# Kernel optimization log

Measured on AMD Instinct MI355X. Metric: run time of the kernel, lower is better.

Reference implementation:

```python
import jax, jax.numpy as jnp
import numpy as np

NUM_HEADS = 16
HEAD_DIM = 64
MAX_TIME = 10000


def apply_rope(x):
    """Interleaved RoPE, faithful to apply_rotary_encoding with the _rope_kernel.

    The NxN kernel maps pairs (x0, x1) -> (-x1, x0); we do it with a reshape
    instead of the dense matmul for efficiency (same math).
    x: [b, t, h, d]
    """
    b, t, h, d = x.shape
    pos = jnp.arange(t, dtype=jnp.float32)                         # [t]
    freq_seq = jnp.arange(d // 2, dtype=jnp.float32) / (d // 2)
    inv_freq = jnp.repeat(jnp.float32(MAX_TIME) ** (-freq_seq), 2)  # [d], interleaved
    theta = pos[:, None] * inv_freq[None, :]                        # [t, d]
    pairs = x.reshape(b, t, h, d // 2, 2)
    x_rot = jnp.stack([-pairs[..., 1], pairs[..., 0]], axis=-1).reshape(b, t, h, d)
    cos = jnp.cos(theta).astype(x.dtype)[None, :, None, :]
    sin = jnp.sin(theta).astype(x.dtype)[None, :, None, :]
    return x * cos + x_rot * sin


def setup_inputs() -> dict:
    key = jax.random.key(0)
    ks = jax.random.split(key, 6)
    B, T, E = 8, 1024, 1024
    H = NUM_HEADS * HEAD_DIM
    s = 0.02  # typical init scale for bias-free Linear weights
    return {
        "inputs_q": jax.random.normal(ks[0], (B, T, E), jnp.float32),
        "inputs_kv": jax.random.normal(ks[1], (B, T, E), jnp.float32),
        "w_q": jax.random.normal(ks[2], (E, H), jnp.float32) * s,
        "w_k": jax.random.normal(ks[3], (E, H), jnp.float32) * s,
        "w_v": jax.random.normal(ks[4], (E, H), jnp.float32) * s,
        "w_o": jax.random.normal(ks[5], (H, E), jnp.float32) * s,
    }


def reference(inputs_q, inputs_kv, w_q, w_k, w_v, w_o):
    b, t, e = inputs_q.shape
    q = (inputs_q @ w_q).reshape(b, t, NUM_HEADS, HEAD_DIM)   # [b,t,h,d]
    k = (inputs_kv @ w_k).reshape(b, -1, NUM_HEADS, HEAD_DIM)  # [b,T,h,d]
    v = (inputs_kv @ w_v).reshape(b, -1, NUM_HEADS, HEAD_DIM)
    q = apply_rope(q)
    k = apply_rope(k)
    logits = jnp.einsum('bthd,bThd->bhtT', q, k) * (1.0 / jnp.sqrt(jnp.float32(HEAD_DIM)))
    attn = jax.nn.softmax(logits, axis=-1)                    # [b,h,t,T]
    out = jnp.einsum('bhtT,bThd->bthd', attn, v).reshape(b, t, NUM_HEADS * HEAD_DIM)
    return out @ w_o                                          # [b,t,e]
```

## Files before the change

kernel.cpp:

```cpp
#include <hip/hip_runtime.h>
#include <math.h>


typedef __attribute__((ext_vector_type(8))) short bf16x8;
typedef __attribute__((ext_vector_type(4))) float f32x4;
typedef __attribute__((ext_vector_type(16))) float f32x16;

__device__ __forceinline__ ushort f2bf(float f) {
    union { float f; uint32_t u; } v; v.f = f;
    uint32_t r = (v.u + 0x7FFF + ((v.u >> 16) & 1)) >> 16;
    return (ushort)r;
}
__device__ __forceinline__ uint cvt_pk_bf16(float a, float b) {
    uint r;
    asm("v_cvt_pk_bf16_f32 %0, %1, %2" : "=v"(r) : "v"(a), "v"(b));
    return r;
}
__device__ __forceinline__ float bf2f(ushort u) {
    union { uint32_t u; float f; } v; v.u = ((uint32_t)u) << 16;
    return v.f;
}

__device__ __forceinline__ void gload16(const ushort* g, ushort* l) {
    __builtin_amdgcn_global_load_lds(
        (const __attribute__((address_space(1))) unsigned int*)g,
        (__attribute__((address_space(3))) unsigned int*)l, 16, 0, 0);
}

__global__ void cast_bf16_2(const float* __restrict__ X0, ushort* __restrict__ Y0,
                            const float* __restrict__ X1, ushort* __restrict__ Y1)
{
    const float* X = blockIdx.y ? X1 : X0;
    ushort* Y = blockIdx.y ? Y1 : Y0;
    int i = blockIdx.x * 256 + threadIdx.x;
    float4 a = ((const float4*)X)[2 * i];
    float4 b = ((const float4*)X)[2 * i + 1];
    union { float4 f; ushort u[8]; } o;
    o.u[0] = f2bf(a.x); o.u[1] = f2bf(a.y); o.u[2] = f2bf(a.z); o.u[3] = f2bf(a.w);
    o.u[4] = f2bf(b.x); o.u[5] = f2bf(b.y); o.u[6] = f2bf(b.z); o.u[7] = f2bf(b.w);
    ((float4*)Y)[i] = o.f;
}

__global__ void transpose_cast_4(const float* __restrict__ w0, ushort* __restrict__ t0,
                                 const float* __restrict__ w1, ushort* __restrict__ t1,
                                 const float* __restrict__ w2, ushort* __restrict__ t2,
                                 const float* __restrict__ w3, ushort* __restrict__ t3)
{
    const int z = blockIdx.z;
    const float* W = (z == 0) ? w0 : (z == 1) ? w1 : (z == 2) ? w2 : w3;
    ushort* Wt = (z == 0) ? t0 : (z == 1) ? t1 : (z == 2) ? t2 : t3;
    __shared__ float t[32][33];
    int bx = blockIdx.x * 32, by = blockIdx.y * 32;
    int tx = threadIdx.x, ty = threadIdx.y;
#pragma unroll
    for (int e = 0; e < 32; e += 8)
        t[ty + e][tx] = W[(size_t)(by + ty + e) * 1024 + bx + tx];
    __syncthreads();
#pragma unroll
    for (int e = 0; e < 32; e += 8)
        Wt[(size_t)(bx + ty + e) * 1024 + by + tx] = f2bf(t[tx][ty + e]);
}

template <bool F32OUT>
__global__ __launch_bounds__(256, 2)
void gemm_bf16(const ushort* __restrict__ A, const ushort* __restrict__ Bt,
               void* __restrict__ C, int M, int N, int K)
{
    __shared__ ushort As[2][128 * 32];
    __shared__ ushort Bs[2][128 * 32];
    const int tid = threadIdx.x;
    const int w = tid >> 6, l = tid & 63;
    const int row0 = blockIdx.x * 128, col0 = blockIdx.y * 128;
    const int wr = (w >> 1) * 64, wc = (w & 1) * 64;

    f32x4 acc[4][4];
#pragma unroll
    for (int i = 0; i < 4; ++i)
#pragma unroll
        for (int j = 0; j < 4; ++j) acc[i][j] = (f32x4)0.f;

    const ushort* Ag = A + (size_t)(row0 + w * 32 + (l >> 2)) * K + (l & 3) * 8;
    const ushort* Bg = Bt + (size_t)(col0 + w * 32 + (l >> 2)) * K + (l & 3) * 8;

    const int arow = (wr + (l & 15)) * 32;
    const int brow = (wc + (l & 15)) * 32;
    const int koff = (l >> 4) * 8;

    auto STAGE = [&](int buf, int kt) {
        ushort* Asw = &As[buf][w * 1024];
        ushort* Bsw = &Bs[buf][w * 1024];
        gload16(Ag + kt, Asw);
        gload16(Ag + 16 * K + kt, Asw + 512);
        gload16(Bg + kt, Bsw);
        gload16(Bg + 16 * K + kt, Bsw + 512);
    };
    auto COMPUTE = [&](int buf) {
        bf16x8 af[4], bfr[4];
#pragma unroll
        for (int fm = 0; fm < 4; ++fm)
            af[fm] = *(const bf16x8*)&As[buf][arow + fm * 512 + koff];
#pragma unroll
        for (int fn = 0; fn < 4; ++fn)
            bfr[fn] = *(const bf16x8*)&Bs[buf][brow + fn * 512 + koff];
#pragma unroll
        for (int fm = 0; fm < 4; ++fm)
#pragma unroll
            for (int fn = 0; fn < 4; ++fn)
                acc[fm][fn] = __builtin_amdgcn_mfma_f32_16x16x32_bf16(
                    af[fm], bfr[fn], acc[fm][fn], 0, 0, 0);
    };

    STAGE(0, 0);
    asm volatile("s_waitcnt vmcnt(0)" ::: "memory");
    __builtin_amdgcn_s_barrier();
    int cur = 0;
    for (int kt = 32; kt < K; kt += 32) {
        STAGE(cur ^ 1, kt);
        COMPUTE(cur);
        asm volatile("s_waitcnt vmcnt(0)" ::: "memory");
        __builtin_amdgcn_s_barrier();
        cur ^= 1;
    }
    COMPUTE(cur);

    const int crow = (l >> 4) * 4;
    const int ccol = l & 15;
#pragma unroll
    for (int fm = 0; fm < 4; ++fm)
#pragma unroll
        for (int fn = 0; fn < 4; ++fn)
#pragma unroll
            for (int r = 0; r < 4; ++r) {
                size_t row = row0 + wr + fm * 16 + crow + r;
                size_t col = col0 + wc + fn * 16 + ccol;
                if (F32OUT)
                    ((float*)C)[row * N + col] = acc[fm][fn][r];
                else
                    ((ushort*)C)[row * N + col] = f2bf(acc[fm][fn][r]);
            }
}

__global__ void rope_bf16_2(ushort* __restrict__ Qb, ushort* __restrict__ Kb)
{
    ushort* X = blockIdx.y ? Kb : Qb;
    const float scale = blockIdx.y ? 1.0f : 0.125f;
    int idx = blockIdx.x * 256 + threadIdx.x;
    int pc = idx & 511;
    int t = (idx >> 9) & 1023;
    int i = pc & 31;
    float inv_freq = exp2f(-(float)i * (13.28771238f / 32.0f));
    float theta = (float)t * inv_freq;
    float s, c;
    sincosf(theta, &s, &c);
    uint32_t v = ((uint32_t*)X)[idx];
    float x0 = bf2f((ushort)(v & 0xffff));
    float x1 = bf2f((ushort)(v >> 16));
    float o0 = (x0 * c - x1 * s) * scale;
    float o1 = (x1 * c + x0 * s) * scale;
    ((uint32_t*)X)[idx] = (uint32_t)f2bf(o0) | ((uint32_t)f2bf(o1) << 16);
}

__global__ __launch_bounds__(256, 4)
void attn_bf16_v2(const ushort* __restrict__ Q, const ushort* __restrict__ K,
                  const ushort* __restrict__ V, ushort* __restrict__ O)
{
    __shared__ uint Ksu[64 * 34];
    __shared__ uint Vtu[64 * 34];
    __shared__ uint Os[4][32 * 36];

    const int tid = threadIdx.x;
    const int w = tid >> 6, l = tid & 63;
    const int lo = l & 31, hi = l >> 5;
    const int bid = blockIdx.x;
    const int qt = bid >> 7;
    const int hb = bid & 127;
    const int h = hb >> 3, b = hb & 7;
    const int colh = h * 64;

    const size_t qrow = (size_t)(b * 1024 + qt * 128 + w * 32 + lo);
    bf16x8 qb[4];
#pragma unroll
    for (int kc = 0; kc < 4; ++kc)
        qb[kc] = *(const bf16x8*)&Q[qrow * 1024 + colh + kc * 16 + hi * 8];

    f32x16 acc[2];
#pragma unroll
    for (int i = 0; i < 2; ++i) acc[i] = (f32x16)0.f;
    float lsum = 0.f;

    const size_t kvbase = (size_t)b * 1024 * 1024 + colh;

    const int skey = tid >> 3, sc = tid & 7;
    const int kp = tid & 31, vg = tid >> 5;

    for (int kt = 0; kt < 16; ++kt) {
        __syncthreads();
#pragma unroll
        for (int u = 0; u < 2; ++u) {
            int key = skey + u * 32;
            uint4 kv = *(const uint4*)&K[kvbase + (size_t)(kt * 64 + key) * 1024 + sc * 8];
            *(uint2*)&Ksu[key * 34 + sc * 4] = make_uint2(kv.x, kv.y);
            *(uint2*)&Ksu[key * 34 + sc * 4 + 2] = make_uint2(kv.z, kv.w);
        }
        {
            uint4 va = *(const uint4*)&V[kvbase + (size_t)(kt * 64 + 2 * kp) * 1024 + vg * 8];
            uint4 vb = *(const uint4*)&V[kvbase + (size_t)(kt * 64 + 2 * kp + 1) * 1024 + vg * 8];
            const ushort* pa = (const ushort*)&va;
            const ushort* pb = (const ushort*)&vb;
#pragma unroll
            for (int e = 0; e < 8; ++e)
                Vtu[(vg * 8 + e) * 34 + kp] = (uint)pa[e] | ((uint)pb[e] << 16);
        }
        __syncthreads();

        uint pw[16];
#pragma unroll
        for (int mt = 0; mt < 2; ++mt) {
            f32x16 s = (f32x16)0.f;
            const int rbase = (mt * 32 + lo) * 34 + hi * 4;
#pragma unroll
            for (int kc = 0; kc < 4; ++kc) {
                union { uint2 d[2]; bf16x8 v; } ak;
                ak.d[0] = *(const uint2*)&Ksu[rbase + kc * 8];
                ak.d[1] = *(const uint2*)&Ksu[rbase + kc * 8 + 2];
                s = __builtin_amdgcn_mfma_f32_32x32x16_bf16(ak.v, qb[kc], s, 0, 0, 0);
            }
            float p[16];
#pragma unroll
            for (int r = 0; r < 16; ++r) {
                p[r] = __expf(s[r]);
                lsum += p[r];
            }
#pragma unroll
            for (int rp = 0; rp < 8; ++rp)
                pw[mt * 8 + rp] = cvt_pk_bf16(p[2 * rp], p[2 * rp + 1]);
        }

        bf16x8 pf[4];
#pragma unroll
        for (int mt = 0; mt < 2; ++mt) {
            uint* W = &pw[mt * 8];
            uint e0 = (uint)__shfl_xor((int)(hi ? W[0] : W[2]), 32);
            uint e1 = (uint)__shfl_xor((int)(hi ? W[1] : W[3]), 32);
            uint e2 = (uint)__shfl_xor((int)(hi ? W[4] : W[6]), 32);
            uint e3 = (uint)__shfl_xor((int)(hi ? W[5] : W[7]), 32);
            union { uint u[4]; bf16x8 v; } f0, f1;
            if (hi == 0) {
                f0.u[0] = W[0]; f0.u[1] = W[1]; f0.u[2] = e0; f0.u[3] = e1;
                f1.u[0] = W[4]; f1.u[1] = W[5]; f1.u[2] = e2; f1.u[3] = e3;
            } else {
                f0.u[0] = e0; f0.u[1] = e1; f0.u[2] = W[2]; f0.u[3] = W[3];
                f1.u[0] = e2; f1.u[1] = e3; f1.u[2] = W[6]; f1.u[3] = W[7];
            }
            pf[mt * 2 + 0] = f0.v;
            pf[mt * 2 + 1] = f1.v;
        }

#pragma unroll
        for (int dmt = 0; dmt < 2; ++dmt) {
            const int rbase = (dmt * 32 + lo) * 34 + hi * 4;
#pragma unroll
            for (int kcg = 0; kcg < 4; ++kcg) {
                union { uint2 d[2]; bf16x8 v; } vk;
                vk.d[0] = *(const uint2*)&Vtu[rbase + kcg * 8];
                vk.d[1] = *(const uint2*)&Vtu[rbase + kcg * 8 + 2];
                acc[dmt] = __builtin_amdgcn_mfma_f32_32x32x16_bf16(vk.v, pf[kcg], acc[dmt], 0, 0, 0);
            }
        }
    }

    float tot = lsum + __shfl_xor(lsum, 32);
    float inv = 1.0f / tot;

    uint* Osw = &Os[w][0];
#pragma unroll
    for (int dmt = 0; dmt < 2; ++dmt)
#pragma unroll
        for (int rp = 0; rp < 8; ++rp) {
            float a0 = acc[dmt][2 * rp] * inv;
            float a1 = acc[dmt][2 * rp + 1] * inv;
            Osw[lo * 36 + dmt * 16 + (rp & 1) + 4 * (rp >> 1) + 2 * hi] =
                cvt_pk_bf16(a0, a1);
        }
    __builtin_amdgcn_s_waitcnt(0);
#pragma unroll
    for (int u = 0; u < 4; ++u) {
        int slot = l + u * 64;
        int qr = slot >> 3, c = slot & 7;
        float4 val = *(const float4*)&Osw[qr * 36 + c * 4];
        *(float4*)&O[(size_t)(b * 1024 + qt * 128 + w * 32 + qr) * 1024 + colh + c * 8] = val;
    }
}

extern "C" void kernel_launch(void* const* d_in, const int* in_sizes, int n_in,
                              void* d_out, int out_size, void* d_ws, size_t ws_size,
                              hipStream_t stream)
{
    const float* xq  = (const float*)d_in[0];
    const float* xkv = (const float*)d_in[1];
    const float* wq  = (const float*)d_in[2];
    const float* wk  = (const float*)d_in[3];
    const float* wv  = (const float*)d_in[4];
    const float* wo  = (const float*)d_in[5];
    float* out = (float*)d_out;

    const int M = 8192, N = 1024, Kd = 1024;
    ushort* Aq  = (ushort*)d_ws;
    ushort* Akv = Aq  + 8388608;
    ushort* WqT = Akv + 8388608;
    ushort* WkT = WqT + 1048576;
    ushort* WvT = WkT + 1048576;
    ushort* WoT = WvT + 1048576;
    ushort* Qb  = WoT + 1048576;
    ushort* Kb  = Qb  + 8388608;
    ushort* Vb  = Kb  + 8388608;
    ushort* Ob  = Vb  + 8388608;

    cast_bf16_2<<<dim3(4096, 2), 256, 0, stream>>>(xq, Aq, xkv, Akv);
    transpose_cast_4<<<dim3(32, 32, 4), dim3(32, 8), 0, stream>>>(
        wq, WqT, wk, WkT, wv, WvT, wo, WoT);

    dim3 gg(M / 128, N / 128);
    gemm_bf16<false><<<gg, 256, 0, stream>>>(Aq,  WqT, Qb, M, N, Kd);
    gemm_bf16<false><<<gg, 256, 0, stream>>>(Akv, WkT, Kb, M, N, Kd);
    gemm_bf16<false><<<gg, 256, 0, stream>>>(Akv, WvT, Vb, M, N, Kd);

    rope_bf16_2<<<dim3(16384, 2), 256, 0, stream>>>(Qb, Kb);

    attn_bf16_v2<<<1024, 256, 0, stream>>>(Qb, Kb, Vb, Ob);

    gemm_bf16<true><<<gg, 256, 0, stream>>>(Ob, WoT, (void*)out, M, N, Kd);
}
```

Measured before the change: 193.1 us.

## Fuse QKV GEMMs into one launch with RoPE epilogue and exp2 softmax

Merges the three Q/K/V projection GEMMs into a single launch over a 3x grid, relying on the transposed weights and outputs being contiguous in the workspace. It applies RoPE and the Q scale (folded with log2e) in the GEMM epilogue using lane shuffles, and the attention kernel switches to exp2f. This removes the separate RoPE pass over Q and K and two kernel launches, and gives the merged GEMM more blocks to fill the device. The cost is extra sincos work in the epilogue and a higher launch-bounds occupancy target.

```diff
diff --git a/kernel.cpp b/kernel.cpp
--- a/kernel.cpp
+++ b/kernel.cpp
@@ -5,6 +5,9 @@
 typedef __attribute__((ext_vector_type(8))) short bf16x8;
 typedef __attribute__((ext_vector_type(4))) float f32x4;
 typedef __attribute__((ext_vector_type(16))) float f32x16;
+
+#define LOG2E 1.44269504f
+#define QSCALE (0.125f * LOG2E)
 
 __device__ __forceinline__ ushort f2bf(float f) {
     union { float f; uint32_t u; } v; v.f = f;
@@ -61,17 +64,22 @@
         Wt[(size_t)(bx + ty + e) * 1024 + by + tx] = f2bf(t[tx][ty + e]);
 }
 
-template <bool F32OUT>
-__global__ __launch_bounds__(256, 2)
-void gemm_bf16(const ushort* __restrict__ A, const ushort* __restrict__ Bt,
-               void* __restrict__ C, int M, int N, int K)
-{
+__global__ __launch_bounds__(256, 4)
+void gemm_qkv(const ushort* __restrict__ Aq, const ushort* __restrict__ Akv,
+              const ushort* __restrict__ Wt, ushort* __restrict__ Out)
+{
+    const int K = 1024, N = 1024;
     __shared__ ushort As[2][128 * 32];
     __shared__ ushort Bs[2][128 * 32];
     const int tid = threadIdx.x;
     const int w = tid >> 6, l = tid & 63;
-    const int row0 = blockIdx.x * 128, col0 = blockIdx.y * 128;
+    const int mat = blockIdx.y >> 3;
+    const int row0 = blockIdx.x * 128, col0 = (blockIdx.y & 7) * 128;
     const int wr = (w >> 1) * 64, wc = (w & 1) * 64;
+
+    const ushort* A = mat ? Akv : Aq;
+    const ushort* Bt = Wt + (size_t)mat * (1024 * 1024);
+    ushort* C = Out + (size_t)mat * 8388608;
 
     f32x4 acc[4][4];
 #pragma unroll
@@ -125,6 +133,34 @@
 
     const int crow = (l >> 4) * 4;
     const int ccol = l & 15;
+
+    if (mat < 2) {
+        const float scale = (mat == 0) ? QSCALE : 1.0f;
+        float invf[4];
+#pragma unroll
+        for (int fn = 0; fn < 4; ++fn) {
+            int i = (fn * 16 + ccol) >> 1;
+            invf[fn] = exp2f(-(float)i * (13.28771238f / 32.0f));
+        }
+        const int odd = ccol & 1;
+#pragma unroll
+        for (int fm = 0; fm < 4; ++fm)
+#pragma unroll
+            for (int r = 0; r < 4; ++r) {
+                int t = (row0 + wr + fm * 16 + crow + r) & 1023;
+#pragma unroll
+                for (int fn = 0; fn < 4; ++fn) {
+                    float x = acc[fm][fn][r];
+                    float partner = __shfl_xor(x, 1, 64);
+                    float sv, cv;
+                    sincosf((float)t * invf[fn], &sv, &cv);
+                    float o = odd ? fmaf(partner, sv, x * cv)
+                                  : fmaf(-partner, sv, x * cv);
+                    acc[fm][fn][r] = o * scale;
+                }
+            }
+    }
+
 #pragma unroll
     for (int fm = 0; fm < 4; ++fm)
 #pragma unroll
@@ -133,31 +169,83 @@
             for (int r = 0; r < 4; ++r) {
                 size_t row = row0 + wr + fm * 16 + crow + r;
                 size_t col = col0 + wc + fn * 16 + ccol;
-                if (F32OUT)
-                    ((float*)C)[row * N + col] = acc[fm][fn][r];
-                else
-                    ((ushort*)C)[row * N + col] = f2bf(acc[fm][fn][r]);
-            }
-}
-
-__global__ void rope_bf16_2(ushort* __restrict__ Qb, ushort* __restrict__ Kb)
-{
-    ushort* X = blockIdx.y ? Kb : Qb;
-    const float scale = blockIdx.y ? 1.0f : 0.125f;
-    int idx = blockIdx.x * 256 + threadIdx.x;
-    int pc = idx & 511;
-    int t = (idx >> 9) & 1023;
-    int i = pc & 31;
-    float inv_freq = exp2f(-(float)i * (13.28771238f / 32.0f));
-    float theta = (float)t * inv_freq;
-    float s, c;
-    sincosf(theta, &s, &c);
-    uint32_t v = ((uint32_t*)X)[idx];
-    float x0 = bf2f((ushort)(v & 0xffff));
-    float x1 = bf2f((ushort)(v >> 16));
-    float o0 = (x0 * c - x1 * s) * scale;
-    float o1 = (x1 * c + x0 * s) * scale;
-    ((uint32_t*)X)[idx] = (uint32_t)f2bf(o0) | ((uint32_t)f2bf(o1) << 16);
+                C[row * N + col] = f2bf(acc[fm][fn][r]);
+            }
+}
+
+__global__ __launch_bounds__(256, 2)
+void gemm_out(const ushort* __restrict__ A, const ushort* __restrict__ Bt,
+              float* __restrict__ C, int M, int N, int K)
+{
+    __shared__ ushort As[2][128 * 32];
+    __shared__ ushort Bs[2][128 * 32];
+    const int tid = threadIdx.x;
+    const int w = tid >> 6, l = tid & 63;
+    const int row0 = blockIdx.x * 128, col0 = blockIdx.y * 128;
+    const int wr = (w >> 1) * 64, wc = (w & 1) * 64;
+
+    f32x4 acc[4][4];
+#pragma unroll
+    for (int i = 0; i < 4; ++i)
+#pragma unroll
+        for (int j = 0; j < 4; ++j) acc[i][j] = (f32x4)0.f;
+
+    const ushort* Ag = A + (size_t)(row0 + w * 32 + (l >> 2)) * K + (l & 3) * 8;
+    const ushort* Bg = Bt + (size_t)(col0 + w * 32 + (l >> 2)) * K + (l & 3) * 8;
+
+    const int arow = (wr + (l & 15)) * 32;
+    const int brow = (wc + (l & 15)) * 32;
+    const int koff = (l >> 4) * 8;
+
+    auto STAGE = [&](int buf, int kt) {
+        ushort* Asw = &As[buf][w * 1024];
+        ushort* Bsw = &Bs[buf][w * 1024];
+        gload16(Ag + kt, Asw);
+        gload16(Ag + 16 * K + kt, Asw + 512);
+        gload16(Bg + kt, Bsw);
+        gload16(Bg + 16 * K + kt, Bsw + 512);
+    };
+    auto COMPUTE = [&](int buf) {
+        bf16x8 af[4], bfr[4];
+#pragma unroll
+        for (int fm = 0; fm < 4; ++fm)
+            af[fm] = *(const bf16x8*)&As[buf][arow + fm * 512 + koff];
+#pragma unroll
+        for (int fn = 0; fn < 4; ++fn)
+            bfr[fn] = *(const bf16x8*)&Bs[buf][brow + fn * 512 + koff];
+#pragma unroll
+        for (int fm = 0; fm < 4; ++fm)
+#pragma unroll
+            for (int fn = 0; fn < 4; ++fn)
+                acc[fm][fn] = __builtin_amdgcn_mfma_f32_16x16x32_bf16(
+                    af[fm], bfr[fn], acc[fm][fn], 0, 0, 0);
+    };
+
+    STAGE(0, 0);
+    asm volatile("s_waitcnt vmcnt(0)" ::: "memory");
+    __builtin_amdgcn_s_barrier();
+    int cur = 0;
+    for (int kt = 32; kt < K; kt += 32) {
+        STAGE(cur ^ 1, kt);
+        COMPUTE(cur);
+        asm volatile("s_waitcnt vmcnt(0)" ::: "memory");
+        __builtin_amdgcn_s_barrier();
+        cur ^= 1;
+    }
+    COMPUTE(cur);
+
+    const int crow = (l >> 4) * 4;
+    const int ccol = l & 15;
+#pragma unroll
+    for (int fm = 0; fm < 4; ++fm)
+#pragma unroll
+        for (int fn = 0; fn < 4; ++fn)
+#pragma unroll
+            for (int r = 0; r < 4; ++r) {
+                size_t row = row0 + wr + fm * 16 + crow + r;
+                size_t col = col0 + wc + fn * 16 + ccol;
+                C[row * N + col] = acc[fm][fn][r];
+            }
 }
 
 __global__ __launch_bounds__(256, 4)
@@ -228,7 +316,7 @@
             float p[16];
 #pragma unroll
             for (int r = 0; r < 16; ++r) {
-                p[r] = __expf(s[r]);
+                p[r] = exp2f(s[r]);
                 lsum += p[r];
             }
 #pragma unroll
@@ -320,14 +408,9 @@
     transpose_cast_4<<<dim3(32, 32, 4), dim3(32, 8), 0, stream>>>(
         wq, WqT, wk, WkT, wv, WvT, wo, WoT);
 
-    dim3 gg(M / 128, N / 128);
-    gemm_bf16<false><<<gg, 256, 0, stream>>>(Aq,  WqT, Qb, M, N, Kd);
-    gemm_bf16<false><<<gg, 256, 0, stream>>>(Akv, WkT, Kb, M, N, Kd);
-    gemm_bf16<false><<<gg, 256, 0, stream>>>(Akv, WvT, Vb, M, N, Kd);
-
-    rope_bf16_2<<<dim3(16384, 2), 256, 0, stream>>>(Qb, Kb);
+    gemm_qkv<<<dim3(64, 24), 256, 0, stream>>>(Aq, Akv, WqT, Qb);
 
     attn_bf16_v2<<<1024, 256, 0, stream>>>(Qb, Kb, Vb, Ob);
 
-    gemm_bf16<true><<<gg, 256, 0, stream>>>(Ob, WoT, (void*)out, M, N, Kd);
-}
+    gemm_out<<<dim3(64, 8), 256, 0, stream>>>(Ob, WoT, out, M, N, Kd);
+}
```

New measurement: 276.8 us. +43.4%, slower.

## Fuse QKV GEMMs with RoPE epilogue, swizzled 2-warp GEMM, exp2 softmax

Applied to the files above, without the earlier changes.

Merges the three projection GEMMs into a single launch and moves RoPE and Q scaling into the GEMM epilogue, with cos/sin read from a precomputed table. This removes the separate rope pass over Q and K and two launches. The GEMM is rewritten as a 128-thread block with an XOR-swizzled LDS layout, a three-stage load-ahead, a grid remap for L2 locality, and each warp holding a 128x64 tile. Folding log2e into the Q scale lets softmax use exp2f. The trade-off is higher register pressure from 32 accumulators per warp, and the epilogue now does shuffles and table reads.

```diff
diff --git a/kernel.cpp b/kernel.cpp
--- a/kernel.cpp
+++ b/kernel.cpp
@@ -5,6 +5,9 @@
 typedef __attribute__((ext_vector_type(8))) short bf16x8;
 typedef __attribute__((ext_vector_type(4))) float f32x4;
 typedef __attribute__((ext_vector_type(16))) float f32x16;
+
+#define LOG2E 1.44269504f
+#define QSCALE (0.125f * LOG2E)
 
 __device__ __forceinline__ ushort f2bf(float f) {
     union { float f; uint32_t u; } v; v.f = f;
@@ -25,6 +28,16 @@
     __builtin_amdgcn_global_load_lds(
         (const __attribute__((address_space(1))) unsigned int*)g,
         (__attribute__((address_space(3))) unsigned int*)l, 16, 0, 0);
+}
+
+__global__ void build_rope_tbl(float2* __restrict__ tbl)
+{
+    int idx = blockIdx.x * 256 + threadIdx.x;
+    int t = idx >> 5, i = idx & 31;
+    float inv_freq = exp2f(-(float)i * (13.28771238f / 32.0f));
+    float s, c;
+    sincosf((float)t * inv_freq, &s, &c);
+    tbl[idx] = make_float2(c, s);
 }
 
 __global__ void cast_bf16_2(const float* __restrict__ X0, ushort* __restrict__ Y0,
@@ -61,49 +74,77 @@
         Wt[(size_t)(bx + ty + e) * 1024 + by + tx] = f2bf(t[tx][ty + e]);
 }
 
-template <bool F32OUT>
-__global__ __launch_bounds__(256, 2)
-void gemm_bf16(const ushort* __restrict__ A, const ushort* __restrict__ Bt,
-               void* __restrict__ C, int M, int N, int K)
-{
-    __shared__ ushort As[2][128 * 32];
-    __shared__ ushort Bs[2][128 * 32];
+template <int MODE>
+__global__ __launch_bounds__(128, 2)
+void gemm8(const ushort* __restrict__ Aq, const ushort* __restrict__ Akv,
+           const ushort* __restrict__ Wt, void* __restrict__ Out,
+           const float2* __restrict__ tbl)
+{
+    const int K = 1024, N = 1024;
+    __shared__ ushort lds[2][8192];
+
     const int tid = threadIdx.x;
     const int w = tid >> 6, l = tid & 63;
-    const int row0 = blockIdx.x * 128, col0 = blockIdx.y * 128;
-    const int wr = (w >> 1) * 64, wc = (w & 1) * 64;
-
-    f32x4 acc[4][4];
-#pragma unroll
-    for (int i = 0; i < 4; ++i)
+
+    const int id = (blockIdx.x & 7) * (gridDim.x >> 3) + (blockIdx.x >> 3);
+    int mat, rt, ct;
+    if (MODE == 0) { mat = id >> 9; int rem = id & 511; rt = rem >> 3; ct = rem & 7; }
+    else           { mat = 0; rt = id >> 3; ct = id & 7; }
+    const int row0 = rt * 128, col0 = ct * 128;
+
+    const ushort* A  = (MODE == 0) ? (mat ? Akv : Aq) : Aq;
+    const ushort* Bt = Wt + (size_t)mat * 1048576;
+
+    const ushort* ag[4];
+    const ushort* bg[4];
+#pragma unroll
+    for (int i = 0; i < 4; ++i) {
+        int D = tid * 16 + i * 2048;
+        int L = D ^ ((D >> 3) & 0x30);
+        int row = L >> 6, colb = L & 63;
+        ag[i] = A  + (size_t)(row0 + row) * K + (colb >> 1);
+        bg[i] = Bt + (size_t)(col0 + row) * K + (colb >> 1);
+    }
+
+    int rdA[8], rdB[4];
+#pragma unroll
+    for (int fm = 0; fm < 8; ++fm) {
+        int byte = (fm * 16 + (l & 15)) * 64 + (l >> 4) * 16;
+        rdA[fm] = (byte ^ ((byte >> 3) & 0x30)) >> 1;
+    }
+#pragma unroll
+    for (int fn = 0; fn < 4; ++fn) {
+        int byte = (w * 64 + fn * 16 + (l & 15)) * 64 + (l >> 4) * 16;
+        rdB[fn] = (byte ^ ((byte >> 3) & 0x30)) >> 1;
+    }
+
+    f32x4 acc[8][4];
+#pragma unroll
+    for (int i = 0; i < 8; ++i)
 #pragma unroll
         for (int j = 0; j < 4; ++j) acc[i][j] = (f32x4)0.f;
 
-    const ushort* Ag = A + (size_t)(row0 + w * 32 + (l >> 2)) * K + (l & 3) * 8;
-    const ushort* Bg = Bt + (size_t)(col0 + w * 32 + (l >> 2)) * K + (l & 3) * 8;
-
-    const int arow = (wr + (l & 15)) * 32;
-    const int brow = (wc + (l & 15)) * 32;
-    const int koff = (l >> 4) * 8;
+    bf16x8 af[8], bfr[4];
 
     auto STAGE = [&](int buf, int kt) {
-        ushort* Asw = &As[buf][w * 1024];
-        ushort* Bsw = &Bs[buf][w * 1024];
-        gload16(Ag + kt, Asw);
-        gload16(Ag + 16 * K + kt, Asw + 512);
-        gload16(Bg + kt, Bsw);
-        gload16(Bg + 16 * K + kt, Bsw + 512);
+        ushort* La = &lds[buf][0];
+#pragma unroll
+        for (int i = 0; i < 4; ++i) {
+            gload16(ag[i] + kt * 32, La + w * 512 + i * 1024);
+            gload16(bg[i] + kt * 32, La + 4096 + w * 512 + i * 1024);
+        }
     };
-    auto COMPUTE = [&](int buf) {
-        bf16x8 af[4], bfr[4];
-#pragma unroll
-        for (int fm = 0; fm < 4; ++fm)
-            af[fm] = *(const bf16x8*)&As[buf][arow + fm * 512 + koff];
+    auto LOADFRAGS = [&](int buf) {
+#pragma unroll
+        for (int fm = 0; fm < 8; ++fm)
+            af[fm] = *(const bf16x8*)&lds[buf][rdA[fm]];
 #pragma unroll
         for (int fn = 0; fn < 4; ++fn)
-            bfr[fn] = *(const bf16x8*)&Bs[buf][brow + fn * 512 + koff];
-#pragma unroll
-        for (int fm = 0; fm < 4; ++fm)
+            bfr[fn] = *(const bf16x8*)&lds[buf][4096 + rdB[fn]];
+    };
+    auto MFMA_ALL = [&]() {
+#pragma unroll
+        for (int fm = 0; fm < 8; ++fm)
 #pragma unroll
             for (int fn = 0; fn < 4; ++fn)
                 acc[fm][fn] = __builtin_amdgcn_mfma_f32_16x16x32_bf16(
@@ -111,53 +152,75 @@
     };
 
     STAGE(0, 0);
+    STAGE(1, 1);
+    asm volatile("s_waitcnt vmcnt(8)" ::: "memory");
+    __builtin_amdgcn_sched_barrier(0);
+    __builtin_amdgcn_s_barrier();
+
+#pragma unroll 2
+    for (int t2 = 0; t2 < 30; ++t2) {
+        const int b = t2 & 1;
+        LOADFRAGS(b);
+        asm volatile("s_waitcnt lgkmcnt(0)" ::: "memory");
+        __builtin_amdgcn_sched_barrier(0);
+        __builtin_amdgcn_s_barrier();
+        STAGE(b, t2 + 2);
+        __builtin_amdgcn_sched_barrier(0);
+        MFMA_ALL();
+        asm volatile("s_waitcnt vmcnt(8)" ::: "memory");
+        __builtin_amdgcn_sched_barrier(0);
+        __builtin_amdgcn_s_barrier();
+    }
+    LOADFRAGS(0);
+    MFMA_ALL();
     asm volatile("s_waitcnt vmcnt(0)" ::: "memory");
+    __builtin_amdgcn_sched_barrier(0);
     __builtin_amdgcn_s_barrier();
-    int cur = 0;
-    for (int kt = 32; kt < K; kt += 32) {
-        STAGE(cur ^ 1, kt);
-        COMPUTE(cur);
-        asm volatile("s_waitcnt vmcnt(0)" ::: "memory");
-        __builtin_amdgcn_s_barrier();
-        cur ^= 1;
-    }
-    COMPUTE(cur);
+    LOADFRAGS(1);
+    MFMA_ALL();
 
     const int crow = (l >> 4) * 4;
     const int ccol = l & 15;
-#pragma unroll
-    for (int fm = 0; fm < 4; ++fm)
+
+    if (MODE == 0 && mat < 2) {
+        const float scale = (mat == 0) ? QSCALE : 1.0f;
+        const int odd = ccol & 1;
+        int ipair[4];
 #pragma unroll
         for (int fn = 0; fn < 4; ++fn)
+            ipair[fn] = ((fn * 16 + ccol) >> 1) & 31;
+#pragma unroll
+        for (int fm = 0; fm < 8; ++fm)
 #pragma unroll
             for (int r = 0; r < 4; ++r) {
-                size_t row = row0 + wr + fm * 16 + crow + r;
-                size_t col = col0 + wc + fn * 16 + ccol;
-                if (F32OUT)
-                    ((float*)C)[row * N + col] = acc[fm][fn][r];
+                int t = (row0 + fm * 16 + crow + r) & 1023;
+                const float2* tb = tbl + (t << 5);
+#pragma unroll
+                for (int fn = 0; fn < 4; ++fn) {
+                    float x = acc[fm][fn][r];
+                    float partner = __shfl_xor(x, 1, 64);
+                    float2 cs = tb[ipair[fn]];
+                    float o = odd ? fmaf(partner, cs.y, x * cs.x)
+                                  : fmaf(-partner, cs.y, x * cs.x);
+                    acc[fm][fn][r] = o * scale;
+                }
+            }
+    }
+
+#pragma unroll
+    for (int fm = 0; fm < 8; ++fm)
+#pragma unroll
+        for (int fn = 0; fn < 4; ++fn)
+#pragma unroll
+            for (int r = 0; r < 4; ++r) {
+                size_t row = row0 + fm * 16 + crow + r;
+                size_t col = col0 + w * 64 + fn * 16 + ccol;
+                if (MODE == 0)
+                    ((ushort*)Out)[(size_t)mat * 8388608 + row * N + col] =
+                        f2bf(acc[fm][fn][r]);
                 else
-                    ((ushort*)C)[row * N + col] = f2bf(acc[fm][fn][r]);
-            }
-}
-
-__global__ void rope_bf16_2(ushort* __restrict__ Qb, ushort* __restrict__ Kb)
-{
-    ushort* X = blockIdx.y ? Kb : Qb;
-    const float scale = blockIdx.y ? 1.0f : 0.125f;
-    int idx = blockIdx.x * 256 + threadIdx.x;
-    int pc = idx & 511;
-    int t = (idx >> 9) & 1023;
-    int i = pc & 31;
-    float inv_freq = exp2f(-(float)i * (13.28771238f / 32.0f));
-    float theta = (float)t * inv_freq;
-    float s, c;
-    sincosf(theta, &s, &c);
-    uint32_t v = ((uint32_t*)X)[idx];
-    float x0 = bf2f((ushort)(v & 0xffff));
-    float x1 = bf2f((ushort)(v >> 16));
-    float o0 = (x0 * c - x1 * s) * scale;
-    float o1 = (x1 * c + x0 * s) * scale;
-    ((uint32_t*)X)[idx] = (uint32_t)f2bf(o0) | ((uint32_t)f2bf(o1) << 16);
+                    ((float*)Out)[row * N + col] = acc[fm][fn][r];
+            }
 }
 
 __global__ __launch_bounds__(256, 4)
@@ -228,7 +291,7 @@
             float p[16];
 #pragma unroll
             for (int r = 0; r < 16; ++r) {
-                p[r] = __expf(s[r]);
+                p[r] = exp2f(s[r]);
                 lsum += p[r];
             }
 #pragma unroll
@@ -304,7 +367,6 @@
     const float* wo  = (const float*)d_in[5];
     float* out = (float*)d_out;
 
-    const int M = 8192, N = 1024, Kd = 1024;
     ushort* Aq  = (ushort*)d_ws;
     ushort* Akv = Aq  + 8388608;
     ushort* WqT = Akv + 8388608;
@@ -315,19 +377,16 @@
     ushort* Kb  = Qb  + 8388608;
     ushort* Vb  = Kb  + 8388608;
     ushort* Ob  = Vb  + 8388608;
-
+    float2* Tbl = (float2*)(Ob + 8388608);
+
+    build_rope_tbl<<<128, 256, 0, stream>>>(Tbl);
     cast_bf16_2<<<dim3(4096, 2), 256, 0, stream>>>(xq, Aq, xkv, Akv);
     transpose_cast_4<<<dim3(32, 32, 4), dim3(32, 8), 0, stream>>>(
         wq, WqT, wk, WkT, wv, WvT, wo, WoT);
 
-    dim3 gg(M / 128, N / 128);
-    gemm_bf16<false><<<gg, 256, 0, stream>>>(Aq,  WqT, Qb, M, N, Kd);
-    gemm_bf16<false><<<gg, 256, 0, stream>>>(Akv, WkT, Kb, M, N, Kd);
-    gemm_bf16<false><<<gg, 256, 0, stream>>>(Akv, WvT, Vb, M, N, Kd);
-
-    rope_bf16_2<<<dim3(16384, 2), 256, 0, stream>>>(Qb, Kb);
+    gemm8<0><<<1536, 128, 0, stream>>>(Aq, Akv, WqT, Qb, Tbl);
 
     attn_bf16_v2<<<1024, 256, 0, stream>>>(Qb, Kb, Vb, Ob);
 
-    gemm_bf16<true><<<gg, 256, 0, stream>>>(Ob, WoT, (void*)out, M, N, Kd);
-}
+    gemm8<1><<<512, 128, 0, stream>>>(Ob, nullptr, WoT, out, Tbl);
+}
```

Result: no change. 191.8 us (-0.7%).
